# Kernel optimization log

Measured on AMD Instinct MI355X. Metric: run time of the kernel, lower is better.

## Reference

```python
import jax, jax.numpy as jnp
import numpy as np

N_EMBD = 1024
N_HEAD = 16
HEAD_DIM = N_EMBD // N_HEAD
SCALE = 1.0 / np.sqrt(HEAD_DIM).astype(np.float32)


def setup_inputs() -> dict:
    key = jax.random.key(0)
    ks = jax.random.split(key, 9)
    B, T = 2, 2048
    std = 1.0 / np.sqrt(N_EMBD).astype(np.float32)
    x = jax.random.normal(ks[0], (B, T, N_EMBD), dtype=jnp.float32)
    Wq = jax.random.normal(ks[1], (N_EMBD, N_EMBD), dtype=jnp.float32) * std
    Wk = jax.random.normal(ks[2], (N_EMBD, N_EMBD), dtype=jnp.float32) * std
    Wv = jax.random.normal(ks[3], (N_EMBD, N_EMBD), dtype=jnp.float32) * std
    Wo = jax.random.normal(ks[4], (N_EMBD, N_EMBD), dtype=jnp.float32) * std
    bq = jax.random.normal(ks[5], (N_EMBD,), dtype=jnp.float32) * 0.01
    bk = jax.random.normal(ks[6], (N_EMBD,), dtype=jnp.float32) * 0.01
    bv = jax.random.normal(ks[7], (N_EMBD,), dtype=jnp.float32) * 0.01
    bo = jax.random.normal(ks[8], (N_EMBD,), dtype=jnp.float32) * 0.01
    return {"x": x, "Wq": Wq, "bq": bq, "Wk": Wk, "bk": bk,
            "Wv": Wv, "bv": bv, "Wo": Wo, "bo": bo}


def reference(x, Wq, bq, Wk, bk, Wv, bv, Wo, bo):
    B, T, C = x.shape
    # project and split heads: (B, H, T, D)
    def heads(y):
        return y.reshape(B, T, N_HEAD, HEAD_DIM).transpose(0, 2, 1, 3)
    q = heads(x @ Wq.T + bq)
    k = heads(x @ Wk.T + bk)
    v = heads(x @ Wv.T + bv)
    # materialized causal attention (matches the torch module's math)
    att = jnp.einsum("bhqd,bhkd->bhqk", q, k) * SCALE
    causal = jnp.tril(jnp.ones((T, T), dtype=bool))
    att = jnp.where(causal, att, -jnp.inf)
    att = jax.nn.softmax(att, axis=-1)
    out = jnp.einsum("bhqk,bhkd->bhqd", att, v)
    out = out.transpose(0, 2, 1, 3).reshape(B, T, C)
    return out @ Wo.T + bo
```

## Files before the change

### kernel.cpp

```cpp
#include <hip/hip_runtime.h>
#include <stdint.h>

typedef unsigned short u16;
typedef __attribute__((ext_vector_type(8))) short short8;
typedef __attribute__((ext_vector_type(4))) float f32x4;
typedef __attribute__((ext_vector_type(16))) float f32x16;

__device__ __forceinline__ u16 f2bf(float f) {
  union { float f; unsigned int u; } c; c.f = f;
  return (u16)((c.u + 0x7FFFu + ((c.u >> 16) & 1u)) >> 16);
}

__device__ __forceinline__ float bf2f(u16 v) {
  union { unsigned int u; float f; } c; c.u = ((unsigned int)v) << 16;
  return c.f;
}

__device__ __forceinline__ f32x4 mfma16(short8 a, short8 b, f32x4 c) {
  return __builtin_amdgcn_mfma_f32_16x16x32_bf16(a, b, c, 0, 0, 0);
}

__device__ __forceinline__ f32x16 mfma32(short8 a, short8 b, f32x16 c) {
  return __builtin_amdgcn_mfma_f32_32x32x16_bf16(a, b, c, 0, 0, 0);
}

__device__ __forceinline__ void gl_lds16(const u16* g, u16* l) {
  __builtin_amdgcn_global_load_lds((const __attribute__((address_space(1))) void*)g,
                                   (__attribute__((address_space(3))) void*)l, 16, 0, 0);
}

__global__ __launch_bounds__(256) void cast_all(
    const float* __restrict__ x, const float* __restrict__ wq, const float* __restrict__ wk,
    const float* __restrict__ wv, const float* __restrict__ wo,
    u16* __restrict__ xb, u16* __restrict__ wqb, u16* __restrict__ wkb,
    u16* __restrict__ wvb, u16* __restrict__ wob) {
  int b = blockIdx.x;
  const float* src; u16* dst; int i;
  if (b < 4096)      { src = x;  dst = xb;  i = b * 256 + threadIdx.x; }
  else if (b < 5120) { src = wq; dst = wqb; i = (b - 4096) * 256 + threadIdx.x; }
  else if (b < 6144) { src = wk; dst = wkb; i = (b - 5120) * 256 + threadIdx.x; }
  else if (b < 7168) { src = wv; dst = wvb; i = (b - 6144) * 256 + threadIdx.x; }
  else               { src = wo; dst = wob; i = (b - 7168) * 256 + threadIdx.x; }
  float4 v = ((const float4*)src)[i];
  ushort4 o;
  o.x = f2bf(v.x); o.y = f2bf(v.y); o.z = f2bf(v.z); o.w = f2bf(v.w);
  ((ushort4*)dst)[i] = o;
}

__global__ __launch_bounds__(256) void qkv_gemm(
    const u16* __restrict__ xb, const u16* __restrict__ wqb, const u16* __restrict__ wkb,
    const u16* __restrict__ wvb, const float* __restrict__ bq, const float* __restrict__ bk,
    const float* __restrict__ bv, u16* __restrict__ Qb, u16* __restrict__ Kb,
    u16* __restrict__ VTb) {
  __shared__ __align__(16) u16 As[128 * 32];
  __shared__ __align__(16) u16 Bs[128 * 32];
  const int id = blockIdx.x;
  const int s = id >> 3;
  const int mblk = (id & 7) + ((s & 3) << 3);
  const int z = (s >> 2) % 3;
  const int nblk = s / 12;
  const u16* __restrict__ W = (z == 0) ? wqb : (z == 1) ? wkb : wvb;
  const float* __restrict__ bias = (z == 0) ? bq : (z == 1) ? bk : bv;
  const int m0 = mblk * 128, n0 = nblk * 128;
  const int tid = threadIdx.x, lane = tid & 63, wave = tid >> 6;
  const int wr = (wave >> 1) * 64, wc = (wave & 1) * 64;
  const int fr = lane & 15, fg = lane >> 4;
  const int lrow = lane >> 2, lcol = (lane & 3) * 8;

  const u16* ga = xb + (size_t)(m0 + wave * 16 + lrow) * 1024 + lcol;
  const u16* gb = W  + (size_t)(n0 + wave * 16 + lrow) * 1024 + lcol;
  u16* la = As + wave * 512;
  u16* lb = Bs + wave * 512;

  f32x4 acc[4][4] = {};

  for (int k0 = 0; k0 < 1024; k0 += 32) {
    gl_lds16(ga + k0, la);
    gl_lds16(ga + 64 * 1024 + k0, la + 2048);
    gl_lds16(gb + k0, lb);
    gl_lds16(gb + 64 * 1024 + k0, lb + 2048);
    __syncthreads();
    short8 a[4], b[4];
#pragma unroll
    for (int i = 0; i < 4; ++i) a[i] = *(const short8*)(As + (wr + i * 16 + fr) * 32 + fg * 8);
#pragma unroll
    for (int i = 0; i < 4; ++i) b[i] = *(const short8*)(Bs + (wc + i * 16 + fr) * 32 + fg * 8);
#pragma unroll
    for (int i = 0; i < 4; ++i)
#pragma unroll
      for (int j = 0; j < 4; ++j) acc[i][j] = mfma16(a[i], b[j], acc[i][j]);
    __syncthreads();
  }

  const float qsc = (z == 0) ? (0.125f * 1.44269504088896f) : 1.0f;
#pragma unroll
  for (int j = 0; j < 4; ++j) {
    const int col = n0 + wc + j * 16 + fr;
    const float bcol = bias[col];
    const int h = col >> 6, d = col & 63;
#pragma unroll
    for (int i = 0; i < 4; ++i) {
#pragma unroll
      for (int r = 0; r < 4; ++r) {
        const int m = m0 + wr + i * 16 + fg * 4 + r;
        const int bi = m >> 11, t = m & 2047;
        const u16 o = f2bf((acc[i][j][r] + bcol) * qsc);
        const size_t bse = (size_t)(bi * 16 + h) << 17;
        if (z == 0)      Qb[bse + (size_t)t * 64 + d] = o;
        else if (z == 1) Kb[bse + (size_t)t * 64 + d] = o;
        else             VTb[bse + (size_t)d * 2048 + t] = o;
      }
    }
  }
}

__global__ __launch_bounds__(256, 2) void attn_kernel(
    const u16* __restrict__ Qb, const u16* __restrict__ Kb, const u16* __restrict__ VTb,
    u16* __restrict__ aOb) {
  __shared__ __align__(16) u16 Ow[4 * 64 * 72];
  __shared__ float Mll[4][2][64];
  const int id = blockIdx.x;
  const int xcd = id & 7, wbl = id >> 3;
  const int cu = wbl & 31, rr = wbl >> 5;
  const int g = cu >> 2;
  const int bh = xcd + ((cu & 3) << 3);
  const int j = (rr == 0) ? 31 - g : (rr == 1) ? 16 + g : (rr == 2) ? 15 - g : g;
  const int tid = threadIdx.x, lane = tid & 63, wave = tid >> 6;
  const int l31 = lane & 31, hi = lane >> 5;
  const size_t base = (size_t)bh << 17;
  const int bi = bh >> 4, h = bh & 15;
  const int q0 = j * 64;

  short8 qf[2][4];
  {
    const u16* qp = Qb + base + (size_t)(q0 + l31) * 64 + hi * 8;
#pragma unroll
    for (int mi = 0; mi < 2; ++mi)
#pragma unroll
      for (int st = 0; st < 4; ++st)
        qf[mi][st] = *(const short8*)(qp + mi * 32 * 64 + st * 16);
  }

  f32x16 oacc[2][2] = {};
  float lrun[2] = {0.f, 0.f};

  for (int ti = wave; ti <= j; ti += 4) {
    const int t0 = ti * 64;
    const u16* kp = Kb + base + (size_t)(t0 + l31) * 64 + hi * 8;
    short8 kf[2][4];
#pragma unroll
    for (int tb = 0; tb < 2; ++tb)
#pragma unroll
      for (int st = 0; st < 4; ++st)
        kf[tb][st] = *(const short8*)(kp + tb * 32 * 64 + st * 16);
    const u16* vp = VTb + base + (size_t)l31 * 2048 + t0 + hi * 8;
    short8 vf[2][2][2];
#pragma unroll
    for (int nb = 0; nb < 2; ++nb)
#pragma unroll
      for (int tb = 0; tb < 2; ++tb)
#pragma unroll
        for (int ks = 0; ks < 2; ++ks)
          vf[nb][tb][ks] = *(const short8*)(vp + (size_t)nb * 32 * 2048 + tb * 32 + ks * 16);

#pragma unroll
    for (int mi = 0; mi < 2; ++mi) {
#pragma unroll
      for (int tb = 0; tb < 2; ++tb) {
        f32x16 s = {};
        __builtin_amdgcn_s_setprio(1);
        s = mfma32(kf[tb][0], qf[mi][0], s);
        s = mfma32(kf[tb][1], qf[mi][1], s);
        s = mfma32(kf[tb][2], qf[mi][2], s);
        s = mfma32(kf[tb][3], qf[mi][3], s);
        __builtin_amdgcn_s_setprio(0);

        if (ti == j) {
          const int qv = mi * 32 + l31;
          const int tbb = tb * 32 + hi * 4;
#pragma unroll
          for (int r = 0; r < 16; ++r) {
            const int tl = tbb + (r & 3) + ((r >> 2) << 3);
            if (tl > qv) s[r] = -1e30f;
          }
        }

        float rs = 0.f;
#pragma unroll
        for (int r = 0; r < 16; ++r) {
          const float pv = exp2f(s[r]);
          s[r] = pv;
          rs += pv;
        }
        lrun[mi] += rs;

        uint32_t w0, w1, w2, w3, w4, w5, w6, w7;
        asm("v_cvt_pk_bf16_f32 %0, %1, %2" : "=v"(w0) : "v"(s[0]),  "v"(s[1]));
        asm("v_cvt_pk_bf16_f32 %0, %1, %2" : "=v"(w1) : "v"(s[2]),  "v"(s[3]));
        asm("v_cvt_pk_bf16_f32 %0, %1, %2" : "=v"(w2) : "v"(s[4]),  "v"(s[5]));
        asm("v_cvt_pk_bf16_f32 %0, %1, %2" : "=v"(w3) : "v"(s[6]),  "v"(s[7]));
        asm("v_cvt_pk_bf16_f32 %0, %1, %2" : "=v"(w4) : "v"(s[8]),  "v"(s[9]));
        asm("v_cvt_pk_bf16_f32 %0, %1, %2" : "=v"(w5) : "v"(s[10]), "v"(s[11]));
        asm("v_cvt_pk_bf16_f32 %0, %1, %2" : "=v"(w6) : "v"(s[12]), "v"(s[13]));
        asm("v_cvt_pk_bf16_f32 %0, %1, %2" : "=v"(w7) : "v"(s[14]), "v"(s[15]));
        asm("v_permlane32_swap_b32 %0, %1" : "+v"(w0), "+v"(w2));
        asm("v_permlane32_swap_b32 %0, %1" : "+v"(w1), "+v"(w3));
        asm("v_permlane32_swap_b32 %0, %1" : "+v"(w4), "+v"(w6));
        asm("v_permlane32_swap_b32 %0, %1" : "+v"(w5), "+v"(w7));
        short8 pa0, pa1;
        {
          uint32_t* p0 = (uint32_t*)&pa0;
          p0[0] = w0; p0[1] = w1; p0[2] = w2; p0[3] = w3;
          uint32_t* p1 = (uint32_t*)&pa1;
          p1[0] = w4; p1[1] = w5; p1[2] = w6; p1[3] = w7;
        }

        __builtin_amdgcn_s_setprio(1);
        oacc[mi][0] = mfma32(pa0, vf[0][tb][0], oacc[mi][0]);
        oacc[mi][0] = mfma32(pa1, vf[0][tb][1], oacc[mi][0]);
        oacc[mi][1] = mfma32(pa0, vf[1][tb][0], oacc[mi][1]);
        oacc[mi][1] = mfma32(pa1, vf[1][tb][1], oacc[mi][1]);
        __builtin_amdgcn_s_setprio(0);
      }
    }
  }

#pragma unroll
  for (int mi = 0; mi < 2; ++mi) Mll[wave][hi][mi * 32 + l31] = lrun[mi];
#pragma unroll
  for (int mi = 0; mi < 2; ++mi)
#pragma unroll
    for (int nb = 0; nb < 2; ++nb)
#pragma unroll
      for (int r = 0; r < 16; ++r) {
        const int q = mi * 32 + (r & 3) + ((r >> 2) << 3) + hi * 4;
        Ow[(wave * 64 + q) * 72 + nb * 32 + l31] = f2bf(oacc[mi][nb][r]);
      }
  __syncthreads();

  const int rq = tid >> 2, c0 = (tid & 3) * 16;
  float lt = 0.f;
#pragma unroll
  for (int w = 0; w < 4; ++w)
#pragma unroll
    for (int gg = 0; gg < 2; ++gg) lt += Mll[w][gg][rq];
  const float inv = __builtin_amdgcn_rcpf(lt);
  float o[16] = {};
#pragma unroll
  for (int w = 0; w < 4; ++w) {
    const u16* orow = &Ow[(w * 64 + rq) * 72 + c0];
    short8 a = *(const short8*)orow;
    short8 b = *(const short8*)(orow + 8);
#pragma unroll
    for (int i = 0; i < 8; ++i) {
      o[i]     += bf2f((u16)a[i]);
      o[8 + i] += bf2f((u16)b[i]);
    }
  }
  short8 r0, r1;
#pragma unroll
  for (int i = 0; i < 8; ++i) {
    r0[i] = (short)f2bf(o[i] * inv);
    r1[i] = (short)f2bf(o[8 + i] * inv);
  }
  u16* op = aOb + ((size_t)bi * 2048 + q0 + rq) * 1024 + h * 64 + c0;
  *(short8*)op = r0;
  *(short8*)(op + 8) = r1;
}

__global__ __launch_bounds__(256) void out_gemm(
    const u16* __restrict__ Ab, const u16* __restrict__ Wb, const float* __restrict__ bo,
    float* __restrict__ out) {
  __shared__ __align__(16) u16 As[128 * 32];
  __shared__ __align__(16) u16 Bs[128 * 32];
  const int id = blockIdx.x;
  const int s = id >> 3;
  const int m0 = ((id & 7) + ((s & 3) << 3)) * 128;
  const int n0 = (s >> 2) * 128;
  const int tid = threadIdx.x, lane = tid & 63, wave = tid >> 6;
  const int wr = (wave >> 1) * 64, wc = (wave & 1) * 64;
  const int fr = lane & 15, fg = lane >> 4;
  const int lrow = lane >> 2, lcol = (lane & 3) * 8;

  const u16* ga = Ab + (size_t)(m0 + wave * 16 + lrow) * 1024 + lcol;
  const u16* gb = Wb + (size_t)(n0 + wave * 16 + lrow) * 1024 + lcol;
  u16* la = As + wave * 512;
  u16* lb = Bs + wave * 512;

  f32x4 acc[4][4] = {};

  for (int k0 = 0; k0 < 1024; k0 += 32) {
    gl_lds16(ga + k0, la);
    gl_lds16(ga + 64 * 1024 + k0, la + 2048);
    gl_lds16(gb + k0, lb);
    gl_lds16(gb + 64 * 1024 + k0, lb + 2048);
    __syncthreads();
    short8 a[4], b[4];
#pragma unroll
    for (int i = 0; i < 4; ++i) a[i] = *(const short8*)(As + (wr + i * 16 + fr) * 32 + fg * 8);
#pragma unroll
    for (int i = 0; i < 4; ++i) b[i] = *(const short8*)(Bs + (wc + i * 16 + fr) * 32 + fg * 8);
#pragma unroll
    for (int i = 0; i < 4; ++i)
#pragma unroll
      for (int j = 0; j < 4; ++j) acc[i][j] = mfma16(a[i], b[j], acc[i][j]);
    __syncthreads();
  }

#pragma unroll
  for (int j = 0; j < 4; ++j) {
    const int col = n0 + wc + j * 16 + fr;
    const float bcol = bo[col];
#pragma unroll
    for (int i = 0; i < 4; ++i)
#pragma unroll
      for (int r = 0; r < 4; ++r) {
        const int m = m0 + wr + i * 16 + fg * 4 + r;
        out[(size_t)m * 1024 + col] = acc[i][j][r] + bcol;
      }
  }
}

extern "C" void kernel_launch(void* const* d_in, const int* in_sizes, int n_in,
                              void* d_out, int out_size, void* d_ws, size_t ws_size,
                              hipStream_t stream) {
  (void)in_sizes; (void)n_in; (void)out_size; (void)ws_size;
  const float* x  = (const float*)d_in[0];
  const float* Wq = (const float*)d_in[1];
  const float* bq = (const float*)d_in[2];
  const float* Wk = (const float*)d_in[3];
  const float* bk = (const float*)d_in[4];
  const float* Wv = (const float*)d_in[5];
  const float* bv = (const float*)d_in[6];
  const float* Wo = (const float*)d_in[7];
  const float* bo = (const float*)d_in[8];
  float* out = (float*)d_out;
  char* ws = (char*)d_ws;

  const size_t MB = 1024 * 1024;
  u16* xb  = (u16*)(ws);
  u16* wqb = (u16*)(ws + 8 * MB);
  u16* wkb = (u16*)(ws + 10 * MB);
  u16* wvb = (u16*)(ws + 12 * MB);
  u16* wob = (u16*)(ws + 14 * MB);
  u16* Qb  = (u16*)(ws + 16 * MB);
  u16* Kb  = (u16*)(ws + 24 * MB);
  u16* VTb = (u16*)(ws + 32 * MB);
  u16* aOb = (u16*)(ws + 40 * MB);

  cast_all<<<8192, 256, 0, stream>>>(x, Wq, Wk, Wv, Wo, xb, wqb, wkb, wvb, wob);
  qkv_gemm<<<768, 256, 0, stream>>>(xb, wqb, wkb, wvb, bq, bk, bv, Qb, Kb, VTb);
  attn_kernel<<<1024, 256, 0, stream>>>(Qb, Kb, VTb, aOb);
  out_gemm<<<256, 256, 0, stream>>>(aOb, wob, bo, out);
}
```

Measured before the change: 116.7 us.

## Stage K/V tiles through swizzled LDS with async prefetch in attention loop

Replaces direct per-lane global loads of K and V^T fragments with global-to-LDS copies into per-wave swizzled buffers. K is double-buffered and the V^T tile is re-staged once its reads finish, so the next tile's fetch overlaps the current tile's MFMA and softmax work. Key tiles shrink from 64 to 32 keys, so each wave runs twice as many smaller iterations. This adds LDS traffic, waitcnt stalls and a block-wide barrier before the epilogue in exchange for more latency hiding. The 48KB shared buffer may also limit occupancy.

Result: faster. 113.1 us (-3.1%).

```diff
diff --git a/kernel.cpp b/kernel.cpp
--- a/kernel.cpp
+++ b/kernel.cpp
@@ -117,8 +117,9 @@
 __global__ __launch_bounds__(256, 2) void attn_kernel(
     const u16* __restrict__ Qb, const u16* __restrict__ Kb, const u16* __restrict__ VTb,
     u16* __restrict__ aOb) {
-  __shared__ __align__(16) u16 Ow[4 * 64 * 72];
+  __shared__ __align__(16) char smem[49152];
   __shared__ float Mll[4][2][64];
+  u16* Ow = (u16*)smem;
   const int id = blockIdx.x;
   const int xcd = id & 7, wbl = id >> 3;
   const int cu = wbl & 31, rr = wbl >> 5;
@@ -131,6 +132,10 @@
   const int bi = bh >> 4, h = bh & 15;
   const int q0 = j * 64;
 
+  u16* kb0 = (u16*)(smem + wave * 12288);
+  u16* kb1 = (u16*)(smem + wave * 12288 + 4096);
+  u16* vb  = (u16*)(smem + wave * 12288 + 8192);
+
   short8 qf[2][4];
   {
     const u16* qp = Qb + base + (size_t)(q0 + l31) * 64 + hi * 8;
@@ -144,43 +149,63 @@
   f32x16 oacc[2][2] = {};
   float lrun[2] = {0.f, 0.f};
 
-  for (int ti = wave; ti <= j; ti += 4) {
-    const int t0 = ti * 64;
-    const u16* kp = Kb + base + (size_t)(t0 + l31) * 64 + hi * 8;
-    short8 kf[2][4];
-#pragma unroll
-    for (int tb = 0; tb < 2; ++tb)
+  auto stageK = [&](int t0, u16* kb) {
+    const u16* kp = Kb + base + (size_t)(t0 + (lane >> 3)) * 64 +
+                    (((lane & 7) ^ ((lane >> 3) & 7)) * 8);
+#pragma unroll
+    for (int i = 0; i < 4; ++i) gl_lds16(kp + (size_t)(8 * i) * 64, kb + i * 512);
+  };
+  auto stageV = [&](int t0) {
+    const u16* vp = VTb + base + (size_t)(lane >> 2) * 2048 + t0 +
+                    (((lane & 3) ^ ((lane >> 2) & 3)) * 8);
+#pragma unroll
+    for (int i = 0; i < 4; ++i) gl_lds16(vp + (size_t)(16 * i) * 2048, vb + i * 512);
+  };
+
+  const int tmax = 2 * j + 1;
+  if (wave <= tmax) {
+    int buf = 0;
+    stageK(wave * 32, kb0);
+    stageV(wave * 32);
+    for (int tu = wave; tu <= tmax; tu += 4) {
+      const int t0 = tu * 32;
+      const bool more = (tu + 4 <= tmax);
+      if (more) {
+        stageK((tu + 4) * 32, buf ? kb0 : kb1);
+        asm volatile("s_waitcnt vmcnt(4)" ::: "memory");
+      } else {
+        asm volatile("s_waitcnt vmcnt(0)" ::: "memory");
+      }
+      __builtin_amdgcn_sched_barrier(0);
+      const char* kb = (const char*)(buf ? kb1 : kb0);
+
+      short8 kf[4];
 #pragma unroll
       for (int st = 0; st < 4; ++st)
-        kf[tb][st] = *(const short8*)(kp + tb * 32 * 64 + st * 16);
-    const u16* vp = VTb + base + (size_t)l31 * 2048 + t0 + hi * 8;
-    short8 vf[2][2][2];
-#pragma unroll
-    for (int nb = 0; nb < 2; ++nb)
-#pragma unroll
-      for (int tb = 0; tb < 2; ++tb)
+        kf[st] = *(const short8*)(kb + l31 * 128 + (((st * 2 + hi) ^ (l31 & 7)) << 4));
+      short8 vf[2][2];
+#pragma unroll
+      for (int nb = 0; nb < 2; ++nb)
 #pragma unroll
         for (int ks = 0; ks < 2; ++ks)
-          vf[nb][tb][ks] = *(const short8*)(vp + (size_t)nb * 32 * 2048 + tb * 32 + ks * 16);
-
-#pragma unroll
-    for (int mi = 0; mi < 2; ++mi) {
-#pragma unroll
-      for (int tb = 0; tb < 2; ++tb) {
+          vf[nb][ks] = *(const short8*)((const char*)vb + (nb * 32 + l31) * 64 +
+                                        (((ks * 2 + hi) ^ (l31 & 3)) << 4));
+
+#pragma unroll
+      for (int mi = 0; mi < 2; ++mi) {
         f32x16 s = {};
         __builtin_amdgcn_s_setprio(1);
-        s = mfma32(kf[tb][0], qf[mi][0], s);
-        s = mfma32(kf[tb][1], qf[mi][1], s);
-        s = mfma32(kf[tb][2], qf[mi][2], s);
-        s = mfma32(kf[tb][3], qf[mi][3], s);
+        s = mfma32(kf[0], qf[mi][0], s);
+        s = mfma32(kf[1], qf[mi][1], s);
+        s = mfma32(kf[2], qf[mi][2], s);
+        s = mfma32(kf[3], qf[mi][3], s);
         __builtin_amdgcn_s_setprio(0);
 
-        if (ti == j) {
-          const int qv = mi * 32 + l31;
-          const int tbb = tb * 32 + hi * 4;
+        if (t0 + 31 > q0 + mi * 32) {
+          const int qv = q0 + mi * 32 + l31;
 #pragma unroll
           for (int r = 0; r < 16; ++r) {
-            const int tl = tbb + (r & 3) + ((r >> 2) << 3);
+            const int tl = t0 + (r & 3) + ((r >> 2) << 3) + hi * 4;
             if (tl > qv) s[r] = -1e30f;
           }
         }
@@ -216,15 +241,23 @@
         }
 
         __builtin_amdgcn_s_setprio(1);
-        oacc[mi][0] = mfma32(pa0, vf[0][tb][0], oacc[mi][0]);
-        oacc[mi][0] = mfma32(pa1, vf[0][tb][1], oacc[mi][0]);
-        oacc[mi][1] = mfma32(pa0, vf[1][tb][0], oacc[mi][1]);
-        oacc[mi][1] = mfma32(pa1, vf[1][tb][1], oacc[mi][1]);
+        oacc[mi][0] = mfma32(pa0, vf[0][0], oacc[mi][0]);
+        oacc[mi][0] = mfma32(pa1, vf[0][1], oacc[mi][0]);
+        oacc[mi][1] = mfma32(pa0, vf[1][0], oacc[mi][1]);
+        oacc[mi][1] = mfma32(pa1, vf[1][1], oacc[mi][1]);
         __builtin_amdgcn_s_setprio(0);
       }
+
+      if (more) {
+        asm volatile("s_waitcnt lgkmcnt(0)" ::: "memory");
+        __builtin_amdgcn_sched_barrier(0);
+        stageV((tu + 4) * 32);
+      }
+      buf ^= 1;
     }
   }
 
+  __syncthreads();
 #pragma unroll
   for (int mi = 0; mi < 2; ++mi) Mll[wave][hi][mi * 32 + l31] = lrun[mi];
 #pragma unroll
```
